# Optimization experiments

Hardware: AMD Instinct MI355X
Metric: run time of the kernel (lower is better)

Reference implementation:

```python
import jax, jax.numpy as jnp
import numpy as np

H, DH, DM = 8, 128, 1024          # n_head, d_head, d_model (n_head*d_head == d_model)
SLEN, BSZ = 256, 64               # slen <= 256 forced by pi0[:, :l]
SCALE = 1.0 / DH ** 0.5
LN_EPS = 1e-5


def setup_inputs() -> dict:
    key = jax.random.key(0)
    k0, k1, k2, k3 = jax.random.split(key, 4)
    h = jax.random.normal(k0, (SLEN, BSZ, DM), jnp.float32)
    W_qkv = jax.random.normal(k1, (H * 4 * DH, DM), jnp.float32) * (DM ** -0.5)
    W_o = jax.random.normal(k2, (DM, H * DH), jnp.float32) * ((H * DH) ** -0.5)
    pi0 = jax.random.uniform(k3, (H, 256), jnp.float32)
    ln_gamma = jnp.ones((DM,), jnp.float32)
    ln_beta = jnp.zeros((DM,), jnp.float32)
    return {"h": h, "W_qkv": W_qkv, "W_o": W_o, "pi0": pi0,
            "ln_gamma": ln_gamma, "ln_beta": ln_beta}


def _phi(x):
    # elu(x)+1 feature map, then L1-normalize over the feature dim
    x = jax.nn.elu(x) + 1.0
    return x / jnp.sum(x, axis=-1, keepdims=True)


def _causal_linear_attn(q, k, v):
    # fast_weight_sum: out_t = sum_{s<=t} (q_t . k_s) v_s  (zero initial fast weights)
    # q,k,v: [b,h,l,d]
    l = q.shape[2]
    scores = jnp.einsum('bhld,bhsd->bhls', q, k)
    mask = jnp.tril(jnp.ones((l, l), dtype=bool))
    scores = jnp.where(mask, scores, jnp.zeros((), scores.dtype))
    return jnp.einsum('bhls,bhsd->bhld', scores, v)


def reference(h, W_qkv, W_o, pi0, ln_gamma, ln_beta):
    l, b, _ = h.shape
    # qkv projection: [l,b,H,4*DH] -> q, k1, k2, v (update_mode='rbf2keys')
    qkv = jnp.einsum('lbm,nm->lbn', h, W_qkv).reshape(l, b, H, 4 * DH)
    q, k1, k2, v = jnp.split(qkv, 4, axis=-1)
    # permute to [b, H, l, d]
    q = _phi(jnp.transpose(q, (1, 2, 0, 3)))
    k1 = _phi(jnp.transpose(k1, (1, 2, 0, 3)))
    k2 = _phi(jnp.transpose(k2, (1, 2, 0, 3)))
    v = jnp.transpose(v, (1, 2, 0, 3))
    # two fast-weight sums (skip_attn_normalization=True path)
    lo1 = _causal_linear_attn(q, k1, v)
    lo2 = _causal_linear_attn(q, k2, v)
    pi = jnp.clip(pi0, 0.0, 1.0)[None, :, :l, None]          # [1,H,l,1]
    layer_out = SCALE * (lo1 * pi + lo2 * (1.0 - pi))         # [b,H,l,d]
    # [b,H,l,d] -> [l,b,H*d]
    layer_out = jnp.transpose(layer_out, (2, 0, 1, 3)).reshape(l, b, H * DH)
    attn_out = jnp.einsum('lbn,mn->lbm', layer_out, W_o)
    # post-LN residual (pre_lnorm=False, dropout=0)
    x = h + attn_out
    mu = jnp.mean(x, axis=-1, keepdims=True)
    var = jnp.mean((x - mu) ** 2, axis=-1, keepdims=True)
    return ln_gamma * (x - mu) / jnp.sqrt(var + LN_EPS) + ln_beta
```

## Files before the change

kernel.cpp:

```cpp
#include <hip/hip_runtime.h>

#define H_     8
#define DM_    1024
#define NQKV_  4096
#define ROWS_  16384
#define PAIRS_ 512
#define SCALE_ 0.08838834764831845f
#define LN_EPS_ 1e-5f

typedef __attribute__((ext_vector_type(8))) short short8;
typedef __attribute__((ext_vector_type(4))) float floatx4;

__device__ __forceinline__ float b2f(unsigned short u) {
  union { unsigned int i; float f; } v; v.i = ((unsigned int)u) << 16; return v.f;
}
__device__ __forceinline__ unsigned short f2b(float f) {
  union { unsigned int i; float f; } v; v.f = f;
  unsigned int b = v.i;
  b += 0x7FFFu + ((b >> 16) & 1u);
  return (unsigned short)(b >> 16);
}

__device__ __forceinline__ void stage_async(const unsigned short* __restrict__ g,
                                            size_t ld, unsigned short* s, int tid) {
#pragma unroll
  for (int p = 0; p < 4; ++p) {
    int idx = p * 256 + tid;
    int r = idx >> 3, j = idx & 7;
    int cg = j ^ (r & 7);
    __builtin_amdgcn_global_load_lds(
        (const __attribute__((address_space(1))) unsigned int*)(g + (size_t)r * ld + cg * 8),
        (__attribute__((address_space(3))) unsigned int*)(s + (size_t)idx * 8),
        16, 0, 0);
  }
}
__device__ __forceinline__ void stage_half(const unsigned short* __restrict__ g,
                                           size_t ld, unsigned short* s, int tid) {
#pragma unroll
  for (int p = 0; p < 2; ++p) {
    int idx = p * 512 + tid;
    int r = idx >> 3, j = idx & 7;
    int cg = j ^ (r & 7);
    __builtin_amdgcn_global_load_lds(
        (const __attribute__((address_space(1))) unsigned int*)(g + (size_t)r * ld + cg * 8),
        (__attribute__((address_space(3))) unsigned int*)(s + (size_t)idx * 8),
        16, 0, 0);
  }
}
__device__ __forceinline__ short8 lds_frag(const unsigned short* s, int row, int cg) {
  return *(const short8*)(s + row * 64 + ((cg ^ (row & 7)) << 3));
}

__global__ __launch_bounds__(256) void cvt_all(const float* __restrict__ h,
                                               const float* __restrict__ wq,
                                               const float* __restrict__ wo,
                                               unsigned short* __restrict__ hb,
                                               unsigned short* __restrict__ wqb,
                                               unsigned short* __restrict__ wob) {
  int i = blockIdx.x * 256 + threadIdx.x;
  const float* src; unsigned short* dst; int off;
  if (i < 2097152)      { src = h;  dst = hb;  off = i; }
  else if (i < 2621440) { src = wq; dst = wqb; off = i - 2097152; }
  else                  { src = wo; dst = wob; off = i - 2621440; }
  const float4* s4 = (const float4*)(src + (size_t)off * 8);
  float4 v0 = s4[0], v1 = s4[1];
  union { short8 v; unsigned short u[8]; } pk;
  pk.u[0] = f2b(v0.x); pk.u[1] = f2b(v0.y); pk.u[2] = f2b(v0.z); pk.u[3] = f2b(v0.w);
  pk.u[4] = f2b(v1.x); pk.u[5] = f2b(v1.y); pk.u[6] = f2b(v1.z); pk.u[7] = f2b(v1.w);
  *(short8*)(dst + (size_t)off * 8) = pk.v;
}

__global__ __launch_bounds__(512, 2) void qkv_gemm(const unsigned short* __restrict__ A,
                                                   const unsigned short* __restrict__ B,
                                                   unsigned short* __restrict__ QKV) {
  __shared__ alignas(16) unsigned short Sh[65536];
  int tid = threadIdx.x;
  int lane = tid & 63, wid = tid >> 6;
  int wm = wid >> 2, wn = wid & 3;
  int quad = lane >> 4, l16 = lane & 15;

  int bid = blockIdx.y * 16 + blockIdx.x;
  int swz = (bid & 7) * 128 + (bid >> 3);
  int bx = swz & 15, by = swz >> 4;
  int n0 = bx * 256, hh = bx >> 1, part0 = (bx & 1) * 2, bb = by;

  const unsigned short* Ab = A + (size_t)bb * DM_;
  const size_t lda = (size_t)64 * DM_;
  const unsigned short* Bb = B + (size_t)n0 * DM_;

  floatx4 acc[8][4];
#pragma unroll
  for (int i = 0; i < 8; ++i)
#pragma unroll
    for (int j = 0; j < 4; ++j)
#pragma unroll
      for (int r = 0; r < 4; ++r) acc[i][j][r] = 0.f;

  stage_half(Ab,                           lda, Sh,         tid);
  stage_half(Ab + (size_t)128 * lda,       lda, Sh + 8192,  tid);
  stage_half(Bb,                           DM_, Sh + 16384, tid);
  stage_half(Bb + (size_t)128 * DM_,       DM_, Sh + 24576, tid);
  stage_half(Ab + 64,                      lda, Sh + 32768, tid);
  stage_half(Ab + (size_t)128 * lda + 64,  lda, Sh + 40960, tid);
  stage_half(Bb + 64,                      DM_, Sh + 49152, tid);
  stage_half(Bb + (size_t)128 * DM_ + 64,  DM_, Sh + 57344, tid);
  asm volatile("s_waitcnt vmcnt(8)" ::: "memory");
  __builtin_amdgcn_s_barrier();

  for (int t = 0; t < 16; ++t) {
    unsigned short* SA = Sh + (t & 1) * 32768;
    unsigned short* SB = SA + 16384;
    short8 a[8], b0[4], b1[4];

#pragma unroll
    for (int m = 0; m < 4; ++m)
#pragma unroll
      for (int kk = 0; kk < 2; ++kk)
        a[m * 2 + kk] = lds_frag(SA, wm * 128 + m * 16 + l16, kk * 4 + quad);
#pragma unroll
    for (int n = 0; n < 2; ++n)
#pragma unroll
      for (int kk = 0; kk < 2; ++kk)
        b0[n * 2 + kk] = lds_frag(SB, wn * 64 + n * 16 + l16, kk * 4 + quad);
    __builtin_amdgcn_s_barrier();
    asm volatile("s_waitcnt lgkmcnt(0)" ::: "memory");
    __builtin_amdgcn_s_setprio(1);
#pragma unroll
    for (int m = 0; m < 4; ++m)
#pragma unroll
      for (int n = 0; n < 2; ++n)
#pragma unroll
        for (int kk = 0; kk < 2; ++kk)
          acc[m][n] = __builtin_amdgcn_mfma_f32_16x16x32_bf16(a[m * 2 + kk], b0[n * 2 + kk], acc[m][n], 0, 0, 0);
    __builtin_amdgcn_s_setprio(0);
    __builtin_amdgcn_s_barrier();

#pragma unroll
    for (int n = 0; n < 2; ++n)
#pragma unroll
      for (int kk = 0; kk < 2; ++kk)
        b1[n * 2 + kk] = lds_frag(SB, wn * 64 + 32 + n * 16 + l16, kk * 4 + quad);
    __builtin_amdgcn_s_barrier();
    asm volatile("s_waitcnt lgkmcnt(0)" ::: "memory");
    __builtin_amdgcn_s_setprio(1);
#pragma unroll
    for (int m = 0; m < 4; ++m)
#pragma unroll
      for (int n = 0; n < 2; ++n)
#pragma unroll
        for (int kk = 0; kk < 2; ++kk)
          acc[m][2 + n] = __builtin_amdgcn_mfma_f32_16x16x32_bf16(a[m * 2 + kk], b1[n * 2 + kk], acc[m][2 + n], 0, 0, 0);
    __builtin_amdgcn_s_setprio(0);
    __builtin_amdgcn_s_barrier();

#pragma unroll
    for (int m = 0; m < 4; ++m)
#pragma unroll
      for (int kk = 0; kk < 2; ++kk)
        a[m * 2 + kk] = lds_frag(SA, wm * 128 + 64 + m * 16 + l16, kk * 4 + quad);
    if (t < 14) {
      size_t kt2 = (size_t)(t + 2) * 64;
      stage_half(Bb + kt2,                      DM_, SB,        tid);
      stage_half(Bb + (size_t)128 * DM_ + kt2,  DM_, SB + 8192, tid);
    }
    __builtin_amdgcn_s_barrier();
    asm volatile("s_waitcnt lgkmcnt(0)" ::: "memory");
    __builtin_amdgcn_s_setprio(1);
#pragma unroll
    for (int m = 0; m < 4; ++m)
#pragma unroll
      for (int n = 0; n < 2; ++n)
#pragma unroll
        for (int kk = 0; kk < 2; ++kk)
          acc[4 + m][n] = __builtin_amdgcn_mfma_f32_16x16x32_bf16(a[m * 2 + kk], b0[n * 2 + kk], acc[4 + m][n], 0, 0, 0);
    __builtin_amdgcn_s_setprio(0);
    __builtin_amdgcn_s_barrier();

    if (t < 14) {
      size_t kt2 = (size_t)(t + 2) * 64;
      stage_half(Ab + kt2,                      lda, SA,        tid);
      stage_half(Ab + (size_t)128 * lda + kt2,  lda, SA + 8192, tid);
    }
    __builtin_amdgcn_s_barrier();
    __builtin_amdgcn_s_setprio(1);
#pragma unroll
    for (int m = 0; m < 4; ++m)
#pragma unroll
      for (int n = 0; n < 2; ++n)
#pragma unroll
        for (int kk = 0; kk < 2; ++kk)
          acc[4 + m][2 + n] = __builtin_amdgcn_mfma_f32_16x16x32_bf16(a[m * 2 + kk], b1[n * 2 + kk], acc[4 + m][2 + n], 0, 0, 0);
    __builtin_amdgcn_s_setprio(0);
    if (t < 14) {
      asm volatile("s_waitcnt vmcnt(8)" ::: "memory");
    } else {
      asm volatile("s_waitcnt vmcnt(0)" ::: "memory");
    }
    __builtin_amdgcn_s_barrier();
  }

  __syncthreads();
  bool isV = (part0 + (wn >> 1)) == 3;
  float* Pf = (float*)Sh;
  float rsum[8][4];
  float inv[8][4];
  if (!isV) {
#pragma unroll
    for (int mt = 0; mt < 8; ++mt)
#pragma unroll
      for (int r = 0; r < 4; ++r) rsum[mt][r] = 0.f;
#pragma unroll
    for (int mt = 0; mt < 8; ++mt)
#pragma unroll
      for (int nt = 0; nt < 4; ++nt)
#pragma unroll
        for (int r = 0; r < 4; ++r) {
          float x = acc[mt][nt][r];
          float f = x > 0.f ? x + 1.f : __expf(x);
          acc[mt][nt][r] = f;
          rsum[mt][r] += f;
        }
#pragma unroll
    for (int off = 1; off < 16; off <<= 1)
#pragma unroll
      for (int mt = 0; mt < 8; ++mt)
#pragma unroll
        for (int r = 0; r < 4; ++r)
          rsum[mt][r] += __shfl_xor(rsum[mt][r], off);
    if (l16 == 0) {
#pragma unroll
      for (int mt = 0; mt < 8; ++mt)
#pragma unroll
        for (int r = 0; r < 4; ++r)
          Pf[(wm * 128 + mt * 16 + quad * 4 + r) * 4 + wn] = rsum[mt][r];
    }
  }
  __syncthreads();
  if (!isV) {
#pragma unroll
    for (int mt = 0; mt < 8; ++mt)
#pragma unroll
      for (int r = 0; r < 4; ++r)
        inv[mt][r] = 1.f / (rsum[mt][r] + Pf[(wm * 128 + mt * 16 + quad * 4 + r) * 4 + (wn ^ 1)]);
  }
  __syncthreads();

#pragma unroll
  for (int h = 0; h < 2; ++h) {
    int part = part0 + h;
    if ((wn >> 1) == h) {
      if (part < 3) {
#pragma unroll
        for (int mt = 0; mt < 8; ++mt)
#pragma unroll
          for (int nt = 0; nt < 4; ++nt)
#pragma unroll
            for (int r = 0; r < 4; ++r) {
              int row = wm * 128 + mt * 16 + quad * 4 + r;
              int col = (wn & 1) * 64 + nt * 16 + l16;
              Sh[row * 136 + col] = f2b(acc[mt][nt][r] * inv[mt][r]);
            }
      } else {
#pragma unroll
        for (int mt = 0; mt < 8; ++mt)
#pragma unroll
          for (int nt = 0; nt < 4; ++nt)
#pragma unroll
            for (int r = 0; r < 4; ++r) {
              int d = (wn & 1) * 64 + nt * 16 + l16;
              int l = wm * 128 + mt * 16 + quad * 4 + r;
              Sh[d * 264 + l] = f2b(acc[mt][nt][r]);
            }
      }
    }
    __syncthreads();
    if (part < 3) {
      unsigned short* P = QKV + (size_t)part * 16777216 + (size_t)(bb * 8 + hh) * 32768;
      int c = tid & 15, g = tid >> 4;
#pragma unroll
      for (int j = 0; j < 8; ++j) {
        int row = j * 32 + g;
        *(short8*)(P + (size_t)row * 128 + c * 8) = *(const short8*)(Sh + row * 136 + c * 8);
      }
    } else {
      unsigned short* Vt = QKV + (size_t)3 * 16777216 + (size_t)(bb * 8 + hh) * 32768;
      int cg = tid & 31, g = tid >> 5;
#pragma unroll
      for (int j = 0; j < 8; ++j) {
        int d = j * 16 + g;
        *(short8*)(Vt + (size_t)d * 256 + cg * 8) = *(const short8*)(Sh + d * 264 + cg * 8);
      }
    }
    __syncthreads();
  }
}

__global__ __launch_bounds__(256) void scores_kernel(const unsigned short* __restrict__ QKV,
                                                     const float* __restrict__ pi0,
                                                     unsigned short* __restrict__ S) {
  __shared__ alignas(16) unsigned short Sh[24576];
  __shared__ float pis[128];
  unsigned short* As  = Sh;
  unsigned short* Bs1 = Sh + 8192;
  unsigned short* Bs2 = Sh + 16384;
  int p = blockIdx.z;
  int hh = p & 7;
  int tid = threadIdx.x;
  int lane = tid & 63, wid = tid >> 6;
  int wm = wid >> 1, wn = wid & 1;
  int quad = lane >> 4, l16 = lane & 15;
  int tix = blockIdx.x;
  int m0 = (tix >= 1) ? 128 : 0;
  int n0 = (tix == 2) ? 128 : 0;
  if (tid < 128) {
    float pv = pi0[hh * 256 + m0 + tid];
    pis[tid] = fminf(fmaxf(pv, 0.f), 1.f);
  }
  const unsigned short* Qb  = QKV + (size_t)p * 32768 + (size_t)m0 * 128;
  const unsigned short* K1b = QKV + 16777216     + (size_t)p * 32768 + (size_t)n0 * 128;
  const unsigned short* K2b = QKV + 2 * 16777216 + (size_t)p * 32768 + (size_t)n0 * 128;

  floatx4 acc1[4][4], acc2[4][4];
#pragma unroll
  for (int i = 0; i < 4; ++i)
#pragma unroll
    for (int j = 0; j < 4; ++j)
#pragma unroll
      for (int r = 0; r < 4; ++r) { acc1[i][j][r] = 0.f; acc2[i][j][r] = 0.f; }

  for (int kt = 0; kt < 128; kt += 64) {
    stage_async(Qb + kt, 128, As, tid);
    stage_async(K1b + kt, 128, Bs1, tid);
    stage_async(K2b + kt, 128, Bs2, tid);
    __syncthreads();
#pragma unroll
    for (int kk = 0; kk < 2; ++kk) {
      short8 af[4], b1[4], b2v[4];
#pragma unroll
      for (int mt = 0; mt < 4; ++mt)
        af[mt] = lds_frag(As, wm * 64 + mt * 16 + l16, kk * 4 + quad);
#pragma unroll
      for (int nt = 0; nt < 4; ++nt) {
        b1[nt]  = lds_frag(Bs1, wn * 64 + nt * 16 + l16, kk * 4 + quad);
        b2v[nt] = lds_frag(Bs2, wn * 64 + nt * 16 + l16, kk * 4 + quad);
      }
#pragma unroll
      for (int mt = 0; mt < 4; ++mt)
#pragma unroll
        for (int nt = 0; nt < 4; ++nt) {
          acc1[mt][nt] = __builtin_amdgcn_mfma_f32_16x16x32_bf16(af[mt], b1[nt],  acc1[mt][nt], 0, 0, 0);
          acc2[mt][nt] = __builtin_amdgcn_mfma_f32_16x16x32_bf16(af[mt], b2v[nt], acc2[mt][nt], 0, 0, 0);
        }
    }
    __syncthreads();
  }
#pragma unroll
  for (int mt = 0; mt < 4; ++mt)
#pragma unroll
    for (int nt = 0; nt < 4; ++nt)
#pragma unroll
      for (int r = 0; r < 4; ++r) {
        int tl = wm * 64 + mt * 16 + quad * 4 + r;
        int sl = wn * 64 + nt * 16 + l16;
        float pv = pis[tl];
        float v = (n0 + sl <= m0 + tl) ? (pv * acc1[mt][nt][r] + (1.f - pv) * acc2[mt][nt][r]) : 0.f;
        Sh[tl * 136 + sl] = f2b(v);
      }
  __syncthreads();
  int c = tid & 15, g = tid >> 4;
#pragma unroll
  for (int j = 0; j < 8; ++j) {
    int r = j * 16 + g;
    size_t gb = (size_t)p * 65536 + (size_t)(m0 + r) * 256 + n0 + c * 8;
    *(short8*)(S + gb) = *(const short8*)(Sh + r * 136 + c * 8);
  }
}

__global__ __launch_bounds__(256, 4) void pv_kernel(const unsigned short* __restrict__ S,
                                                    const unsigned short* __restrict__ Vt,
                                                    unsigned short* __restrict__ LO) {
  __shared__ alignas(16) unsigned short Sh[17408];
  unsigned short* As = Sh;
  unsigned short* Bs = Sh + 8192;
  int p = blockIdx.z;
  int b = p >> 3, hh = p & 7;
  int tid = threadIdx.x;
  int lane = tid & 63, wid = tid >> 6;
  int wm = wid >> 1, wn = wid & 1;
  int quad = lane >> 4, l16 = lane & 15;
  int m0 = blockIdx.y * 128;
  int kEnd = (blockIdx.y == 0) ? 128 : 256;
  const unsigned short* Ab = S  + (size_t)p * 65536 + (size_t)m0 * 256;
  const unsigned short* Bb = Vt + (size_t)p * 32768;

  floatx4 acc[4][4];
#pragma unroll
  for (int i = 0; i < 4; ++i)
#pragma unroll
    for (int j = 0; j < 4; ++j)
#pragma unroll
      for (int r = 0; r < 4; ++r) acc[i][j][r] = 0.f;

  for (int kt = 0; kt < kEnd; kt += 64) {
    stage_async(Ab + kt, 256, As, tid);
    stage_async(Bb + kt, 256, Bs, tid);
    __syncthreads();
#pragma unroll
    for (int kk = 0; kk < 2; ++kk) {
      short8 af[4], bfv[4];
#pragma unroll
      for (int mt = 0; mt < 4; ++mt)
        af[mt] = lds_frag(As, wm * 64 + mt * 16 + l16, kk * 4 + quad);
#pragma unroll
      for (int nt = 0; nt < 4; ++nt)
        bfv[nt] = lds_frag(Bs, wn * 64 + nt * 16 + l16, kk * 4 + quad);
#pragma unroll
      for (int mt = 0; mt < 4; ++mt)
#pragma unroll
        for (int nt = 0; nt < 4; ++nt)
          acc[mt][nt] = __builtin_amdgcn_mfma_f32_16x16x32_bf16(af[mt], bfv[nt], acc[mt][nt], 0, 0, 0);
    }
    __syncthreads();
  }
#pragma unroll
  for (int mt = 0; mt < 4; ++mt)
#pragma unroll
    for (int nt = 0; nt < 4; ++nt)
#pragma unroll
      for (int r = 0; r < 4; ++r) {
        int tl = wm * 64 + mt * 16 + quad * 4 + r;
        int d = wn * 64 + nt * 16 + l16;
        Sh[tl * 136 + d] = f2b(SCALE_ * acc[mt][nt][r]);
      }
  __syncthreads();
  int c = tid & 15, g = tid >> 4;
#pragma unroll
  for (int j = 0; j < 8; ++j) {
    int r = j * 16 + g;
    int t = m0 + r;
    size_t gb = ((size_t)t * 64 + b) * 1024 + hh * 128 + c * 8;
    *(short8*)(LO + gb) = *(const short8*)(Sh + r * 136 + c * 8);
  }
}

__global__ __launch_bounds__(256, 4) void wo_gemm(const unsigned short* __restrict__ A,
                                                  const unsigned short* __restrict__ B,
                                                  const float* __restrict__ hin,
                                                  float* __restrict__ X) {
  __shared__ alignas(16) unsigned short As[128 * 64], Bs[128 * 64];
  int tid = threadIdx.x;
  int lane = tid & 63, wid = tid >> 6;
  int wm = wid >> 1, wn = wid & 1;
  int quad = lane >> 4, l16 = lane & 15;
  int m0 = blockIdx.y * 128, n0 = blockIdx.x * 128;
  const unsigned short* Ab = A + (size_t)m0 * DM_;
  const unsigned short* Bb = B + (size_t)n0 * DM_;

  floatx4 acc[4][4];
#pragma unroll
  for (int i = 0; i < 4; ++i)
#pragma unroll
    for (int j = 0; j < 4; ++j)
#pragma unroll
      for (int r = 0; r < 4; ++r) acc[i][j][r] = 0.f;

  for (int kt = 0; kt < DM_; kt += 64) {
    stage_async(Ab + kt, DM_, As, tid);
    stage_async(Bb + kt, DM_, Bs, tid);
    __syncthreads();
#pragma unroll
    for (int kk = 0; kk < 2; ++kk) {
      short8 af[4], bfv[4];
#pragma unroll
      for (int mt = 0; mt < 4; ++mt)
        af[mt] = lds_frag(As, wm * 64 + mt * 16 + l16, kk * 4 + quad);
#pragma unroll
      for (int nt = 0; nt < 4; ++nt)
        bfv[nt] = lds_frag(Bs, wn * 64 + nt * 16 + l16, kk * 4 + quad);
#pragma unroll
      for (int mt = 0; mt < 4; ++mt)
#pragma unroll
        for (int nt = 0; nt < 4; ++nt)
          acc[mt][nt] = __builtin_amdgcn_mfma_f32_16x16x32_bf16(af[mt], bfv[nt], acc[mt][nt], 0, 0, 0);
    }
    __syncthreads();
  }
#pragma unroll
  for (int mt = 0; mt < 4; ++mt)
#pragma unroll
    for (int nt = 0; nt < 4; ++nt)
#pragma unroll
      for (int r = 0; r < 4; ++r) {
        int row = m0 + wm * 64 + mt * 16 + quad * 4 + r;
        int col = n0 + wn * 64 + nt * 16 + l16;
        size_t idx = (size_t)row * DM_ + col;
        X[idx] = acc[mt][nt][r] + hin[idx];
      }
}

__global__ __launch_bounds__(256) void ln_kernel(float* __restrict__ X,
                                                 const float* __restrict__ gamma,
                                                 const float* __restrict__ beta) {
  int row = blockIdx.x;
  int tid = threadIdx.x;
  float* x = X + (size_t)row * DM_;
  float4 v = *(const float4*)(x + tid * 4);
  float s  = v.x + v.y + v.z + v.w;
  float ss = v.x * v.x + v.y * v.y + v.z * v.z + v.w * v.w;
#pragma unroll
  for (int off = 32; off; off >>= 1) {
    s  += __shfl_down(s, off);
    ss += __shfl_down(ss, off);
  }
  __shared__ float rs[4], rss[4];
  int wv = tid >> 6, lane = tid & 63;
  if (lane == 0) { rs[wv] = s; rss[wv] = ss; }
  __syncthreads();
  float St  = rs[0] + rs[1] + rs[2] + rs[3];
  float SSt = rss[0] + rss[1] + rss[2] + rss[3];
  float mu = St * (1.f / DM_);
  float var = SSt * (1.f / DM_) - mu * mu;
  float rstd = rsqrtf(var + LN_EPS_);
  float4 o;
#pragma unroll
  for (int j = 0; j < 4; ++j) {
    int c = tid * 4 + j;
    (&o.x)[j] = gamma[c] * ((&v.x)[j] - mu) * rstd + beta[c];
  }
  *(float4*)(x + tid * 4) = o;
}

extern "C" void kernel_launch(void* const* d_in, const int* in_sizes, int n_in,
                              void* d_out, int out_size, void* d_ws, size_t ws_size,
                              hipStream_t stream) {
  const float* h     = (const float*)d_in[0];
  const float* Wqkv  = (const float*)d_in[1];
  const float* Wo    = (const float*)d_in[2];
  const float* pi0   = (const float*)d_in[3];
  const float* gamma = (const float*)d_in[4];
  const float* beta  = (const float*)d_in[5];
  char* ws = (char*)d_ws;

  unsigned short* QKV   = (unsigned short*)ws;
  unsigned short* Sbuf  = (unsigned short*)(ws + 134217728ull);
  unsigned short* hb    = (unsigned short*)(ws + 134217728ull);
  unsigned short* Wqkvb = (unsigned short*)(ws + 167772160ull);
  unsigned short* Wob   = (unsigned short*)(ws + 201326592ull);
  unsigned short* LO    = (unsigned short*)ws;
  float* X = (float*)d_out;

  dim3 blk(256);
  cvt_all<<<dim3(10752), blk, 0, stream>>>(h, Wqkv, Wo, hb, Wqkvb, Wob);
  qkv_gemm<<<dim3(16, 64, 1), dim3(512), 0, stream>>>(hb, Wqkvb, QKV);
  scores_kernel<<<dim3(3, 1, PAIRS_), blk, 0, stream>>>(QKV, pi0, Sbuf);
  pv_kernel<<<dim3(1, 2, PAIRS_), blk, 0, stream>>>(Sbuf, QKV + (size_t)3 * 16777216, LO);
  wo_gemm<<<dim3(DM_ / 128, ROWS_ / 128, 1), blk, 0, stream>>>(LO, Wob, h, X);
  ln_kernel<<<dim3(ROWS_, 1, 1), blk, 0, stream>>>(X, gamma, beta);
}
```

Measured before the change: 445.0 us.

## Restructure QKV GEMM pipeline with one-tile-ahead B prefetch and precomputed offsets

Rewrites the QKV GEMM main loop as a 2x-unrolled macro body that alternates LDS buffers. The B tile is now prefetched one step ahead instead of two, while A stays two ahead. Staging addresses and LDS fragment pointers are computed once outside the loop, and the MFMA quadrants run in a snake order. This aims to cut per-iteration address arithmetic and the time spent waiting on loads, and the added sched_barriers pin the instruction schedule. The cost is a shorter B prefetch distance, more register pressure, and an extra B fragment reload per tile.

```diff
diff --git a/kernel.cpp b/kernel.cpp
--- a/kernel.cpp
+++ b/kernel.cpp
@@ -34,18 +34,15 @@
         16, 0, 0);
   }
 }
-__device__ __forceinline__ void stage_half(const unsigned short* __restrict__ g,
-                                           size_t ld, unsigned short* s, int tid) {
-#pragma unroll
-  for (int p = 0; p < 2; ++p) {
-    int idx = p * 512 + tid;
-    int r = idx >> 3, j = idx & 7;
-    int cg = j ^ (r & 7);
-    __builtin_amdgcn_global_load_lds(
-        (const __attribute__((address_space(1))) unsigned int*)(g + (size_t)r * ld + cg * 8),
-        (__attribute__((address_space(3))) unsigned int*)(s + (size_t)idx * 8),
-        16, 0, 0);
-  }
+__device__ __forceinline__ void stage_h(const unsigned short* __restrict__ g,
+                                        size_t o0, size_t o1,
+                                        unsigned short* s, int lo0, int lo1) {
+  __builtin_amdgcn_global_load_lds(
+      (const __attribute__((address_space(1))) unsigned int*)(g + o0),
+      (__attribute__((address_space(3))) unsigned int*)(s + lo0), 16, 0, 0);
+  __builtin_amdgcn_global_load_lds(
+      (const __attribute__((address_space(1))) unsigned int*)(g + o1),
+      (__attribute__((address_space(3))) unsigned int*)(s + lo1), 16, 0, 0);
 }
 __device__ __forceinline__ short8 lds_frag(const unsigned short* s, int row, int cg) {
   return *(const short8*)(s + row * 64 + ((cg ^ (row & 7)) << 3));
@@ -78,6 +75,7 @@
   int lane = tid & 63, wid = tid >> 6;
   int wm = wid >> 2, wn = wid & 3;
   int quad = lane >> 4, l16 = lane & 15;
+  int s7 = l16 & 7;
 
   int bid = blockIdx.y * 16 + blockIdx.x;
   int swz = (bid & 7) * 128 + (bid >> 3);
@@ -86,7 +84,17 @@
 
   const unsigned short* Ab = A + (size_t)bb * DM_;
   const size_t lda = (size_t)64 * DM_;
+  const unsigned short* AbH = Ab + (size_t)128 * lda;
   const unsigned short* Bb = B + (size_t)n0 * DM_;
+  const unsigned short* BbH = Bb + (size_t)128 * DM_;
+
+  int r0 = tid >> 3, jj = tid & 7;
+  int cg = jj ^ (r0 & 7);
+  size_t oA0 = (size_t)r0 * lda + cg * 8;
+  size_t oA1 = (size_t)(r0 + 64) * lda + cg * 8;
+  size_t oB0 = (size_t)r0 * DM_ + cg * 8;
+  size_t oB1 = (size_t)(r0 + 64) * DM_ + cg * 8;
+  int lo0 = tid * 8, lo1 = 4096 + tid * 8;
 
   floatx4 acc[8][4];
 #pragma unroll
@@ -96,108 +104,119 @@
 #pragma unroll
       for (int r = 0; r < 4; ++r) acc[i][j][r] = 0.f;
 
-  stage_half(Ab,                           lda, Sh,         tid);
-  stage_half(Ab + (size_t)128 * lda,       lda, Sh + 8192,  tid);
-  stage_half(Bb,                           DM_, Sh + 16384, tid);
-  stage_half(Bb + (size_t)128 * DM_,       DM_, Sh + 24576, tid);
-  stage_half(Ab + 64,                      lda, Sh + 32768, tid);
-  stage_half(Ab + (size_t)128 * lda + 64,  lda, Sh + 40960, tid);
-  stage_half(Bb + 64,                      DM_, Sh + 49152, tid);
-  stage_half(Bb + (size_t)128 * DM_ + 64,  DM_, Sh + 57344, tid);
-  asm volatile("s_waitcnt vmcnt(8)" ::: "memory");
+  stage_h(Ab,        oA0, oA1, Sh,         lo0, lo1);
+  stage_h(AbH,       oA0, oA1, Sh + 8192,  lo0, lo1);
+  stage_h(Bb,        oB0, oB1, Sh + 16384, lo0, lo1);
+  stage_h(BbH,       oB0, oB1, Sh + 24576, lo0, lo1);
+  stage_h(Ab + 64,   oA0, oA1, Sh + 32768, lo0, lo1);
+  stage_h(AbH + 64,  oA0, oA1, Sh + 40960, lo0, lo1);
+  asm volatile("s_waitcnt vmcnt(4)" ::: "memory");
   __builtin_amdgcn_s_barrier();
 
-  for (int t = 0; t < 16; ++t) {
-    unsigned short* SA = Sh + (t & 1) * 32768;
-    unsigned short* SB = SA + 16384;
-    short8 a[8], b0[4], b1[4];
-
-#pragma unroll
-    for (int m = 0; m < 4; ++m)
-#pragma unroll
-      for (int kk = 0; kk < 2; ++kk)
-        a[m * 2 + kk] = lds_frag(SA, wm * 128 + m * 16 + l16, kk * 4 + quad);
-#pragma unroll
-    for (int n = 0; n < 2; ++n)
-#pragma unroll
-      for (int kk = 0; kk < 2; ++kk)
-        b0[n * 2 + kk] = lds_frag(SB, wn * 64 + n * 16 + l16, kk * 4 + quad);
-    __builtin_amdgcn_s_barrier();
-    asm volatile("s_waitcnt lgkmcnt(0)" ::: "memory");
-    __builtin_amdgcn_s_setprio(1);
-#pragma unroll
-    for (int m = 0; m < 4; ++m)
-#pragma unroll
-      for (int n = 0; n < 2; ++n)
-#pragma unroll
-        for (int kk = 0; kk < 2; ++kk)
-          acc[m][n] = __builtin_amdgcn_mfma_f32_16x16x32_bf16(a[m * 2 + kk], b0[n * 2 + kk], acc[m][n], 0, 0, 0);
-    __builtin_amdgcn_s_setprio(0);
-    __builtin_amdgcn_s_barrier();
-
-#pragma unroll
-    for (int n = 0; n < 2; ++n)
-#pragma unroll
-      for (int kk = 0; kk < 2; ++kk)
-        b1[n * 2 + kk] = lds_frag(SB, wn * 64 + 32 + n * 16 + l16, kk * 4 + quad);
-    __builtin_amdgcn_s_barrier();
-    asm volatile("s_waitcnt lgkmcnt(0)" ::: "memory");
-    __builtin_amdgcn_s_setprio(1);
-#pragma unroll
-    for (int m = 0; m < 4; ++m)
-#pragma unroll
-      for (int n = 0; n < 2; ++n)
-#pragma unroll
-        for (int kk = 0; kk < 2; ++kk)
-          acc[m][2 + n] = __builtin_amdgcn_mfma_f32_16x16x32_bf16(a[m * 2 + kk], b1[n * 2 + kk], acc[m][2 + n], 0, 0, 0);
-    __builtin_amdgcn_s_setprio(0);
-    __builtin_amdgcn_s_barrier();
-
-#pragma unroll
-    for (int m = 0; m < 4; ++m)
-#pragma unroll
-      for (int kk = 0; kk < 2; ++kk)
-        a[m * 2 + kk] = lds_frag(SA, wm * 128 + 64 + m * 16 + l16, kk * 4 + quad);
-    if (t < 14) {
-      size_t kt2 = (size_t)(t + 2) * 64;
-      stage_half(Bb + kt2,                      DM_, SB,        tid);
-      stage_half(Bb + (size_t)128 * DM_ + kt2,  DM_, SB + 8192, tid);
-    }
-    __builtin_amdgcn_s_barrier();
-    asm volatile("s_waitcnt lgkmcnt(0)" ::: "memory");
-    __builtin_amdgcn_s_setprio(1);
-#pragma unroll
-    for (int m = 0; m < 4; ++m)
-#pragma unroll
-      for (int n = 0; n < 2; ++n)
-#pragma unroll
-        for (int kk = 0; kk < 2; ++kk)
-          acc[4 + m][n] = __builtin_amdgcn_mfma_f32_16x16x32_bf16(a[m * 2 + kk], b0[n * 2 + kk], acc[4 + m][n], 0, 0, 0);
-    __builtin_amdgcn_s_setprio(0);
-    __builtin_amdgcn_s_barrier();
-
-    if (t < 14) {
-      size_t kt2 = (size_t)(t + 2) * 64;
-      stage_half(Ab + kt2,                      lda, SA,        tid);
-      stage_half(Ab + (size_t)128 * lda + kt2,  lda, SA + 8192, tid);
-    }
-    __builtin_amdgcn_s_barrier();
-    __builtin_amdgcn_s_setprio(1);
-#pragma unroll
-    for (int m = 0; m < 4; ++m)
-#pragma unroll
-      for (int n = 0; n < 2; ++n)
-#pragma unroll
-        for (int kk = 0; kk < 2; ++kk)
-          acc[4 + m][2 + n] = __builtin_amdgcn_mfma_f32_16x16x32_bf16(a[m * 2 + kk], b1[n * 2 + kk], acc[4 + m][2 + n], 0, 0, 0);
-    __builtin_amdgcn_s_setprio(0);
-    if (t < 14) {
-      asm volatile("s_waitcnt vmcnt(8)" ::: "memory");
-    } else {
-      asm volatile("s_waitcnt vmcnt(0)" ::: "memory");
-    }
-    __builtin_amdgcn_s_barrier();
-  }
+#define TILE_BODY(T, BUF, OBUF)                                                \
+  {                                                                            \
+    unsigned short* SB = (BUF) + 16384;                                        \
+    const unsigned short* aA0 = (BUF) + (wm * 128 + l16) * 64 + ((0 ^ (quad ^ s7)) ? 0 : 0) + ((quad ^ s7) << 3); \
+    const unsigned short* aA1 = (BUF) + (wm * 128 + l16) * 64 + (((4 + quad) ^ s7) << 3); \
+    const unsigned short* bA0 = SB + (wn * 64 + l16) * 64 + ((quad ^ s7) << 3);\
+    const unsigned short* bA1 = SB + (wn * 64 + l16) * 64 + (((4 + quad) ^ s7) << 3); \
+    short8 a[8], b[4];                                                         \
+                   \
+    if ((T) < 15) {                                                            \
+      size_t kn = (size_t)((T) + 1) * 64;                                      \
+      stage_h(Bb + kn,  oB0, oB1, (OBUF) + 16384, lo0, lo1);                   \
+      stage_h(BbH + kn, oB0, oB1, (OBUF) + 24576, lo0, lo1);                   \
+    }                                                                          \
+    _Pragma("unroll")                                                          \
+    for (int mt = 0; mt < 4; ++mt) {                                           \
+      a[mt * 2 + 0] = *(const short8*)(aA0 + mt * 1024);                       \
+      a[mt * 2 + 1] = *(const short8*)(aA1 + mt * 1024);                       \
+    }                                                                          \
+    _Pragma("unroll")                                                          \
+    for (int nt = 0; nt < 2; ++nt) {                                           \
+      b[nt * 2 + 0] = *(const short8*)(bA0 + nt * 1024);                       \
+      b[nt * 2 + 1] = *(const short8*)(bA1 + nt * 1024);                       \
+    }                                                                          \
+    __builtin_amdgcn_sched_barrier(0);                                         \
+    __builtin_amdgcn_s_barrier();                                              \
+    __builtin_amdgcn_s_setprio(1);                                             \
+    _Pragma("unroll")                                                          \
+    for (int kk = 0; kk < 2; ++kk)                                             \
+      _Pragma("unroll")                                                        \
+      for (int m = 0; m < 4; ++m)                                              \
+        _Pragma("unroll")                                                      \
+        for (int n = 0; n < 2; ++n)                                            \
+          acc[m][n] = __builtin_amdgcn_mfma_f32_16x16x32_bf16(a[m * 2 + kk], b[n * 2 + kk], acc[m][n], 0, 0, 0); \
+    __builtin_amdgcn_s_setprio(0);                                             \
+    __builtin_amdgcn_s_barrier();                                              \
+                                                 \
+    _Pragma("unroll")                                                          \
+    for (int nt = 0; nt < 2; ++nt) {                                           \
+      b[nt * 2 + 0] = *(const short8*)(bA0 + 2048 + nt * 1024);                \
+      b[nt * 2 + 1] = *(const short8*)(bA1 + 2048 + nt * 1024);                \
+    }                                                                          \
+    __builtin_amdgcn_sched_barrier(0);                                         \
+    __builtin_amdgcn_s_barrier();                                              \
+    __builtin_amdgcn_s_setprio(1);                                             \
+    _Pragma("unroll")                                                          \
+    for (int kk = 0; kk < 2; ++kk)                                             \
+      _Pragma("unroll")                                                        \
+      for (int m = 0; m < 4; ++m)                                              \
+        _Pragma("unroll")                                                      \
+        for (int n = 0; n < 2; ++n)                                            \
+          acc[m][2 + n] = __builtin_amdgcn_mfma_f32_16x16x32_bf16(a[m * 2 + kk], b[n * 2 + kk], acc[m][2 + n], 0, 0, 0); \
+    __builtin_amdgcn_s_setprio(0);                                             \
+    __builtin_amdgcn_s_barrier();                                              \
+                                       \
+    _Pragma("unroll")                                                          \
+    for (int mt = 0; mt < 4; ++mt) {                                           \
+      a[mt * 2 + 0] = *(const short8*)(aA0 + 4096 + mt * 1024);                \
+      a[mt * 2 + 1] = *(const short8*)(aA1 + 4096 + mt * 1024);                \
+    }                                                                          \
+    __builtin_amdgcn_sched_barrier(0);                                         \
+    __builtin_amdgcn_s_barrier();                                              \
+    __builtin_amdgcn_s_setprio(1);                                             \
+    _Pragma("unroll")                                                          \
+    for (int kk = 0; kk < 2; ++kk)                                             \
+      _Pragma("unroll")                                                        \
+      for (int m = 0; m < 4; ++m)                                              \
+        _Pragma("unroll")                                                      \
+        for (int n = 0; n < 2; ++n)                                            \
+          acc[4 + m][2 + n] = __builtin_amdgcn_mfma_f32_16x16x32_bf16(a[m * 2 + kk], b[n * 2 + kk], acc[4 + m][2 + n], 0, 0, 0); \
+    __builtin_amdgcn_s_setprio(0);                                             \
+    __builtin_amdgcn_s_barrier();                                              \
+                \
+    if ((T) < 14) {                                                            \
+      size_t kt2 = (size_t)((T) + 2) * 64;                                     \
+      stage_h(Ab + kt2,  oA0, oA1, (BUF),        lo0, lo1);                    \
+      stage_h(AbH + kt2, oA0, oA1, (BUF) + 8192, lo0, lo1);                    \
+    }                                                                          \
+    _Pragma("unroll")                                                          \
+    for (int nt = 0; nt < 2; ++nt) {                                           \
+      b[nt * 2 + 0] = *(const short8*)(bA0 + nt * 1024);                       \
+      b[nt * 2 + 1] = *(const short8*)(bA1 + nt * 1024);                       \
+    }                                                                          \
+    __builtin_amdgcn_sched_barrier(0);                                         \
+    __builtin_amdgcn_s_barrier();                                              \
+    __builtin_amdgcn_s_setprio(1);                                             \
+    _Pragma("unroll")                                                          \
+    for (int kk = 0; kk < 2; ++kk)                                             \
+      _Pragma("unroll")                                                        \
+      for (int m = 0; m < 4; ++m)                                              \
+        _Pragma("unroll")                                                      \
+        for (int n = 0; n < 2; ++n)                                            \
+          acc[4 + m][n] = __builtin_amdgcn_mfma_f32_16x16x32_bf16(a[m * 2 + kk], b[n * 2 + kk], acc[4 + m][n], 0, 0, 0); \
+    __builtin_amdgcn_s_setprio(0);                                             \
+    if ((T) < 14) { asm volatile("s_waitcnt vmcnt(4)" ::: "memory"); }         \
+    else          { asm volatile("s_waitcnt vmcnt(0)" ::: "memory"); }         \
+    __builtin_amdgcn_s_barrier();                                              \
+  }
+
+  for (int t = 0; t < 16; t += 2) {
+    TILE_BODY(t,     Sh,         Sh + 32768)
+    TILE_BODY(t + 1, Sh + 32768, Sh)
+  }
+#undef TILE_BODY
 
   __syncthreads();
   bool isV = (part0 + (wn >> 1)) == 3;
@@ -284,11 +303,11 @@
       }
     } else {
       unsigned short* Vt = QKV + (size_t)3 * 16777216 + (size_t)(bb * 8 + hh) * 32768;
-      int cg = tid & 31, g = tid >> 5;
+      int cg2 = tid & 31, g = tid >> 5;
 #pragma unroll
       for (int j = 0; j < 8; ++j) {
         int d = j * 16 + g;
-        *(short8*)(Vt + (size_t)d * 256 + cg * 8) = *(const short8*)(Sh + d * 264 + cg * 8);
+        *(short8*)(Vt + (size_t)d * 256 + cg2 * 8) = *(const short8*)(Sh + d * 264 + cg2 * 8);
       }
     }
     __syncthreads();
```

New measurement: 438.7 us. No clear change (-1.4%).
